# Optimization experiments

Hardware: AMD Instinct MI355X
Metric: run time of the kernel (lower is better)

## Reference

```python
import jax, jax.numpy as jnp
import numpy as np
import math

PS = 65          # patch_size
NB_ANG = 8       # num_ang_bins
NB_SP = 4        # num_spatial_bins
CLIP = 0.2
EPS = 1e-10
BIN_KS = 2 * (PS // (NB_SP + 1))   # 26
BIN_STRIDE = PS // NB_SP           # 16
BIN_PAD = BIN_KS // 4              # 6


def _gaussian_kernel2d(ks, sigma):
    x = jnp.arange(ks, dtype=jnp.float32) - ks // 2
    if ks % 2 == 0:
        x = x + 0.5
    g = jnp.exp(-(x * x) / (2.0 * sigma * sigma))
    g = g / g.sum()
    return jnp.outer(g, g)  # [ps, ps]


def _sift_pooling_kernel(ks):
    ks2 = ks / 2.0
    xc2 = ks2 - jnp.abs(jnp.arange(ks, dtype=jnp.float32) + 0.5 - ks2)
    return jnp.outer(xc2, xc2) / (ks2 * ks2)  # [26, 26] triangular bilinear kernel


def _l2n(x):
    # torch F.normalize(p=2, dim=-1, eps=1e-12)
    return x / jnp.maximum(jnp.linalg.norm(x, axis=-1, keepdims=True), 1e-12)


def setup_inputs() -> dict:
    key = jax.random.key(0)
    image_batch = jax.random.uniform(key, (16, 3, 520, 520), dtype=jnp.float32)
    return {"image_batch": image_batch}


def reference(image_batch):
    B, C, H, W = image_batch.shape
    nH, nW = H // PS, W // PS
    # torch unfold(2,ps,ps).unfold(3,ps,ps).reshape(-1, c, ps, ps)
    # (row-major reshape replicated exactly, including its channel/patch mixing)
    p = image_batch.reshape(B, C, nH, PS, nW, PS).transpose(0, 1, 2, 4, 3, 5)
    x = p.reshape(-1, C, PS, PS)  # [N, C, ps, ps]; (N,C) treated as independent patches
    N = x.shape[0]

    # kornia spatial_gradient(mode='diff', normalized=True): replicate pad, central diff / 2
    xp = jnp.pad(x, ((0, 0), (0, 0), (1, 1), (1, 1)), mode='edge')
    gx = (xp[:, :, 1:-1, 2:] - xp[:, :, 1:-1, :-2]) * 0.5
    gy = (xp[:, :, 2:, 1:-1] - xp[:, :, :-2, 1:-1]) * 0.5

    mag = jnp.sqrt(gx * gx + gy * gy + EPS)
    ori = jnp.arctan2(gy, gx + EPS) + 2.0 * jnp.pi
    gk = _gaussian_kernel2d(PS, PS / math.sqrt(2.0))
    mag = mag * gk  # Gaussian spatial weighting

    # soft orientation binning
    o_big = (NB_ANG / (2.0 * jnp.pi)) * ori
    bo0f = jnp.floor(o_big)
    wo1 = o_big - bo0f
    bo0 = (bo0f % NB_ANG).astype(jnp.int32)
    bo1 = (bo0 + 1) % NB_ANG
    # [N, C, ps, ps, 8] soft histogram field
    contrib = (jax.nn.one_hot(bo0, NB_ANG, dtype=x.dtype) * ((1.0 - wo1) * mag)[..., None]
               + jax.nn.one_hot(bo1, NB_ANG, dtype=x.dtype) * (wo1 * mag)[..., None])

    # spatial pooling: conv 26x26, stride 16, zero-pad 6 -> 4x4 per angle bin
    contrib = jnp.moveaxis(contrib, -1, 2).reshape(N * C * NB_ANG, 1, PS, PS)
    pk = _sift_pooling_kernel(BIN_KS)[None, None]  # [1,1,26,26]
    pooled = jax.lax.conv_general_dilated(
        contrib, pk,
        window_strides=(BIN_STRIDE, BIN_STRIDE),
        padding=((BIN_PAD, BIN_PAD), (BIN_PAD, BIN_PAD)),
        dimension_numbers=('NCHW', 'OIHW', 'NCHW'))  # [N*C*8, 1, 4, 4]

    desc = pooled.reshape(N, C, NB_ANG * NB_SP * NB_SP)  # [N, C, 128]
    desc = _l2n(desc)
    desc = jnp.clip(desc, 0.0, CLIP)
    desc = _l2n(desc)
    return desc  # [B*nH*nW, C, 128] (root_sift=False)
```

## Files before the change

### kernel.cpp

```cpp
#include <hip/hip_runtime.h>
#include <math.h>

#define PSTR 33

__device__ __forceinline__ float fast_atan2f(float y, float x) {
    float ax = fabsf(x), ay = fabsf(y);
    float mx = fmaxf(ax, ay);
    float mn = fminf(ax, ay);
    float a = mn * __builtin_amdgcn_rcpf(fmaxf(mx, 1e-30f));
    float s = a * a;
    float r = fmaf(s, fmaf(s, fmaf(s, fmaf(s, fmaf(s, -0.0117212f, 0.05265332f),
                    -0.11643287f), 0.19354346f), -0.33262347f), 0.99997726f) * a;
    r = (ay > ax) ? (1.57079637f - r) : r;
    r = (x < 0.0f) ? (3.14159274f - r) : r;
    return copysignf(r, y);
}

#define WGT(SY, RR) ((13.0f - fabsf((float)(RR) - 16.0f * (SY) - 6.5f)) * (1.0f / 13.0f))

#define FMA8(P, W)                                                        \
    P##0 = fmaf(s0, (W), P##0); P##1 = fmaf(s1, (W), P##1);               \
    P##2 = fmaf(s2, (W), P##2); P##3 = fmaf(s3, (W), P##3);               \
    P##4 = fmaf(s4, (W), P##4); P##5 = fmaf(s5, (W), P##5);               \
    P##6 = fmaf(s6, (W), P##6); P##7 = fmaf(s7, (W), P##7);

#define RDL(RR) __uint_as_float((unsigned)__builtin_amdgcn_readlane((int)__float_as_uint(G), (RR)))

#define PIX(ARR, I, RR, ACCUM)                                            \
    {                                                                     \
        float grow = ((RR) < 64) ? RDL((RR) & 63) : g64;                  \
        float gw = grow * GC;                                             \
        float c64r = c64buf[(RR) + 1];                                    \
        float xc = ARR[I];                                                \
        float xl = __shfl_up(xc, 1, 64);   if (lane == 0)  xl = xc;       \
        float xr = __shfl_down(xc, 1, 64); if (lane == 63) xr = c64r;     \
        float dx = xr - xl;                                               \
        float dy = ARR[(I) + 1] - ARR[(I) - 1];                           \
        float magw = sqrtf(fmaf(dx, dx, fmaf(dy, dy, 4e-10f))) * gw;      \
        float ang = fast_atan2f(dy, dx + 2e-10f);                         \
        float o = fmaf(ang, 1.27323954f, 8.0f);                           \
        int bi = (int)o;                                                  \
        float wo1 = o - (float)bi;                                        \
        int bn0 = bi & 7;                                                 \
        int bn1 = (bi + 1) & 7;                                           \
        float q1 = wo1 * magw;                                            \
        float q0 = magw - q1;                                             \
        float s0 = (bn0 == 0) ? q0 : ((bn1 == 0) ? q1 : 0.0f);            \
        float s1 = (bn0 == 1) ? q0 : ((bn1 == 1) ? q1 : 0.0f);            \
        float s2 = (bn0 == 2) ? q0 : ((bn1 == 2) ? q1 : 0.0f);            \
        float s3 = (bn0 == 3) ? q0 : ((bn1 == 3) ? q1 : 0.0f);            \
        float s4 = (bn0 == 4) ? q0 : ((bn1 == 4) ? q1 : 0.0f);            \
        float s5 = (bn0 == 5) ? q0 : ((bn1 == 5) ? q1 : 0.0f);            \
        float s6 = (bn0 == 6) ? q0 : ((bn1 == 6) ? q1 : 0.0f);            \
        float s7 = (bn0 == 7) ? q0 : ((bn1 == 7) ? q1 : 0.0f);            \
        ACCUM                                                             \
    }

#define LOAD_RA(BASE)                                                     \
    _Pragma("unroll")                                                     \
    for (int i = 0; i < 18; ++i) {                                        \
        int rr = (BASE) + i; rr = (rr < 0) ? 0 : ((rr > 64) ? 64 : rr);   \
        RA[i] = src[rr * 520 + lane];                                     \
    }
#define LOAD_RB(BASE)                                                     \
    _Pragma("unroll")                                                     \
    for (int i = 0; i < 19; ++i) {                                        \
        int rr = (BASE) + i; rr = (rr < 0) ? 0 : ((rr > 64) ? 64 : rr);   \
        RB[i] = src[rr * 520 + lane];                                     \
    }
#define PIN_RA  _Pragma("unroll") for (int i = 0; i < 18; ++i) asm volatile("" : "+v"(RA[i]));
#define PIN_RB  _Pragma("unroll") for (int i = 0; i < 19; ++i) asm volatile("" : "+v"(RB[i]));

__global__ __launch_bounds__(64)
__attribute__((amdgpu_waves_per_eu(2, 3)))
void sift_kernel(const float* __restrict__ in, float* __restrict__ out) {
    __shared__ float part[65 * PSTR];
    __shared__ float c64buf[67];

    const int lane = threadIdx.x;
    const int m  = blockIdx.x;
    const int bc = m >> 6;
    const int ij = m & 63;
    const float* src = in + (size_t)bc * (520 * 520) + (ij >> 3) * (65 * 520) + (ij & 7) * 65;

    {
        int rr = lane - 1; rr = (rr < 0) ? 0 : rr;
        c64buf[lane] = src[rr * 520 + 64];
        if (lane < 3) {
            int r2 = 63 + lane; r2 = (r2 > 64) ? 64 : r2;
            c64buf[64 + lane] = src[r2 * 520 + 64];
        }
        if (lane < 32) part[64 * PSTR + lane] = 0.0f;
    }
    float xl63  = src[lane * 520 + 63];
    float xl63b = src[64 * 520 + 63];

    float RA[18], RB[19];
    LOAD_RA(-1)
    LOAD_RB(15)

    float dd = (float)(lane - 32);
    float E  = __expf(-(dd * dd) * (1.0f / 4225.0f));
    float ssum = E;
    #pragma unroll
    for (int off = 32; off > 0; off >>= 1) ssum += __shfl_xor(ssum, off, 64);
    const float e64 = __expf(-1024.0f / 4225.0f);
    float inv = 1.0f / (ssum + e64);
    float G   = E * inv;
    float g64 = e64 * inv;
    const float GC = 0.5f * G;

    const int cb = lane * PSTR;

    float A0=0,A1=0,A2=0,A3=0,A4=0,A5=0,A6=0,A7=0;
    float B0=0,B1=0,B2=0,B3=0,B4=0,B5=0,B6=0,B7=0;
    float C0=0,C1=0,C2=0,C3=0,C4=0,C5=0,C6=0,C7=0;
    float F0=0,F1=0,F2=0,F3=0,F4=0,F5=0,F6=0,F7=0;

    PIN_RA
    #pragma unroll
    for (int r = 0; r < 10; ++r)   PIX(RA, r + 1, r, FMA8(A, WGT(0, r)))
    #pragma unroll
    for (int r = 10; r < 16; ++r)  PIX(RA, r + 1, r, FMA8(A, WGT(0, r)) FMA8(B, WGT(1, r)))

    LOAD_RA(31)
    PIN_RB
    #pragma unroll
    for (int r = 16; r < 20; ++r)  PIX(RB, r - 15, r, FMA8(A, WGT(0, r)) FMA8(B, WGT(1, r)))
    #pragma unroll
    for (int r = 20; r < 26; ++r)  PIX(RB, r - 15, r, FMA8(B, WGT(1, r)))
    #pragma unroll
    for (int r = 26; r < 32; ++r)  PIX(RB, r - 15, r, FMA8(B, WGT(1, r)) FMA8(C, WGT(2, r)))
    part[cb + 0] = A0; part[cb + 1] = A1; part[cb + 2] = A2; part[cb + 3] = A3;
    part[cb + 4] = A4; part[cb + 5] = A5; part[cb + 6] = A6; part[cb + 7] = A7;

    LOAD_RB(47)
    PIN_RA
    #pragma unroll
    for (int r = 32; r < 36; ++r)  PIX(RA, r - 31, r, FMA8(B, WGT(1, r)) FMA8(C, WGT(2, r)))
    #pragma unroll
    for (int r = 36; r < 42; ++r)  PIX(RA, r - 31, r, FMA8(C, WGT(2, r)))
    #pragma unroll
    for (int r = 42; r < 48; ++r)  PIX(RA, r - 31, r, FMA8(C, WGT(2, r)) FMA8(F, WGT(3, r)))
    part[cb + 8] = B0; part[cb + 9] = B1; part[cb +10] = B2; part[cb +11] = B3;
    part[cb +12] = B4; part[cb +13] = B5; part[cb +14] = B6; part[cb +15] = B7;

    PIN_RB
    #pragma unroll
    for (int r = 48; r < 52; ++r)  PIX(RB, r - 47, r, FMA8(C, WGT(2, r)) FMA8(F, WGT(3, r)))
    #pragma unroll
    for (int r = 52; r < 65; ++r)  PIX(RB, r - 47, r, FMA8(F, WGT(3, r)))
    part[cb +16] = C0; part[cb +17] = C1; part[cb +18] = C2; part[cb +19] = C3;
    part[cb +20] = C4; part[cb +21] = C5; part[cb +22] = C6; part[cb +23] = C7;
    part[cb +24] = F0; part[cb +25] = F1; part[cb +26] = F2; part[cb +27] = F3;
    part[cb +28] = F4; part[cb +29] = F5; part[cb +30] = F6; part[cb +31] = F7;

    {
        int r = lane;
        float xu  = c64buf[r];
        float xcc = c64buf[r + 1];
        float xd  = c64buf[r + 2];
        float dx = xcc - xl63;
        float dy = xd - xu;
        float magw = sqrtf(fmaf(dx, dx, fmaf(dy, dy, 4e-10f))) * (G * (0.5f * g64));
        float ang = fast_atan2f(dy, dx + 2e-10f);
        float o   = fmaf(ang, 1.27323954f, 8.0f);
        int bi = (int)o;
        float wo1 = o - (float)bi;
        int b0 = bi & 7;
        int b1 = (bi + 1) & 7;
        float q1 = wo1 * magw;
        float q0 = magw - q1;
        float* eb = &part[64 * PSTR];
        int syA = (r + 6) >> 4; if (syA > 3) syA = 3;
        float uA = (float)(r - 16 * syA + 6);
        float wA = (13.0f - fabsf(uA - 12.5f)) * (1.0f / 13.0f);
        atomicAdd(eb + syA * 8 + b0, q0 * wA);
        atomicAdd(eb + syA * 8 + b1, q1 * wA);
        int syB = syA - 1;
        if (syB >= 0) {
            float uB = (float)(r - 16 * syB + 6);
            float wB = (13.0f - fabsf(uB - 12.5f)) * (1.0f / 13.0f);
            if (wB > 0.0f) {
                atomicAdd(eb + syB * 8 + b0, q0 * wB);
                atomicAdd(eb + syB * 8 + b1, q1 * wB);
            }
        }
        if (lane == 0) {
            float xu2  = c64buf[64];
            float xc2  = c64buf[65];
            float xd2  = c64buf[66];
            float dx2 = xc2 - xl63b;
            float dy2 = xd2 - xu2;
            float mg = sqrtf(fmaf(dx2, dx2, fmaf(dy2, dy2, 4e-10f))) * (g64 * (0.5f * g64));
            float an = fast_atan2f(dy2, dx2 + 2e-10f);
            float o2 = fmaf(an, 1.27323954f, 8.0f);
            int bi2 = (int)o2;
            float w1 = o2 - (float)bi2;
            int c0 = bi2 & 7;
            int c1 = (bi2 + 1) & 7;
            float p1 = w1 * mg;
            float p0 = mg - p1;
            const float w64 = 3.5f * (1.0f / 13.0f);
            atomicAdd(eb + 3 * 8 + c0, p0 * w64);
            atomicAdd(eb + 3 * 8 + c1, p1 * w64);
        }
    }

    {
        float v0, v1;
        #pragma unroll
        for (int h = 0; h < 2; ++h) {
            int o  = lane + h * 64;
            int a  = o >> 4;
            int sy = (o >> 2) & 3;
            int sx = o & 3;
            float s = 0.0f;
            #pragma unroll 2
            for (int k = 0; k < 26; ++k) {
                int c = sx * 16 - 6 + k;
                if ((unsigned)c <= 64u) {
                    float wc = (13.0f - fabsf((float)k - 12.5f)) * (1.0f / 13.0f);
                    s = fmaf(wc, part[c * PSTR + sy * 8 + a], s);
                }
            }
            if (h == 0) v0 = s; else v1 = s;
        }
        float ss = v0 * v0 + v1 * v1;
        #pragma unroll
        for (int off = 32; off > 0; off >>= 1) ss += __shfl_xor(ss, off, 64);
        float sc = 1.0f / fmaxf(sqrtf(ss), 1e-12f);
        v0 = fminf(fmaxf(v0 * sc, 0.0f), 0.2f);
        v1 = fminf(fmaxf(v1 * sc, 0.0f), 0.2f);
        ss = v0 * v0 + v1 * v1;
        #pragma unroll
        for (int off = 32; off > 0; off >>= 1) ss += __shfl_xor(ss, off, 64);
        sc = 1.0f / fmaxf(sqrtf(ss), 1e-12f);
        out[(size_t)m * 128 + lane]      = v0 * sc;
        out[(size_t)m * 128 + lane + 64] = v1 * sc;
    }
}

extern "C" void kernel_launch(void* const* d_in, const int* in_sizes, int n_in,
                              void* d_out, int out_size, void* d_ws, size_t ws_size,
                              hipStream_t stream) {
    const float* in = (const float*)d_in[0];
    float* out = (float*)d_out;
    sift_kernel<<<3072, 64, 0, stream>>>(in, out);
}
```

Measured before the change: 49.50 us.

## Split patch rows across two wavefronts per block with shared partial histograms

```diff
diff --git a/kernel.cpp b/kernel.cpp
--- a/kernel.cpp
+++ b/kernel.cpp
@@ -1,7 +1,7 @@
 #include <hip/hip_runtime.h>
 #include <math.h>
 
-#define PSTR 33
+#define PSTR 57
 
 __device__ __forceinline__ float fast_atan2f(float y, float x) {
     float ax = fabsf(x), ay = fabsf(y);
@@ -56,48 +56,49 @@
         ACCUM                                                             \
     }
 
-#define LOAD_RA(BASE)                                                     \
-    _Pragma("unroll")                                                     \
-    for (int i = 0; i < 18; ++i) {                                        \
-        int rr = (BASE) + i; rr = (rr < 0) ? 0 : ((rr > 64) ? 64 : rr);   \
-        RA[i] = src[rr * 520 + lane];                                     \
-    }
-#define LOAD_RB(BASE)                                                     \
-    _Pragma("unroll")                                                     \
-    for (int i = 0; i < 19; ++i) {                                        \
-        int rr = (BASE) + i; rr = (rr < 0) ? 0 : ((rr > 64) ? 64 : rr);   \
-        RB[i] = src[rr * 520 + lane];                                     \
-    }
 #define PIN_RA  _Pragma("unroll") for (int i = 0; i < 18; ++i) asm volatile("" : "+v"(RA[i]));
 #define PIN_RB  _Pragma("unroll") for (int i = 0; i < 19; ++i) asm volatile("" : "+v"(RB[i]));
 
-__global__ __launch_bounds__(64)
-__attribute__((amdgpu_waves_per_eu(2, 3)))
+__global__ __launch_bounds__(128)
+__attribute__((amdgpu_waves_per_eu(4)))
 void sift_kernel(const float* __restrict__ in, float* __restrict__ out) {
     __shared__ float part[65 * PSTR];
     __shared__ float c64buf[67];
-
-    const int lane = threadIdx.x;
+    __shared__ float ssbuf[4];
+
+    const int tid  = threadIdx.x;
+    const int lane = tid & 63;
+    const int wid  = tid >> 6;
     const int m  = blockIdx.x;
     const int bc = m >> 6;
     const int ij = m & 63;
     const float* src = in + (size_t)bc * (520 * 520) + (ij >> 3) * (65 * 520) + (ij & 7) * 65;
 
-    {
-        int rr = lane - 1; rr = (rr < 0) ? 0 : rr;
-        c64buf[lane] = src[rr * 520 + 64];
-        if (lane < 3) {
-            int r2 = 63 + lane; r2 = (r2 > 64) ? 64 : r2;
-            c64buf[64 + lane] = src[r2 * 520 + 64];
-        }
-        if (lane < 32) part[64 * PSTR + lane] = 0.0f;
-    }
-    float xl63  = src[lane * 520 + 63];
-    float xl63b = src[64 * 520 + 63];
+    if (tid < 67) {
+        int rr = tid - 1; rr = (rr < 0) ? 0 : ((rr > 64) ? 64 : rr);
+        c64buf[tid] = src[rr * 520 + 64];
+    }
+    for (int k = tid; k < 65 * 8; k += 128) {
+        part[(k >> 3) * PSTR + 48 + (k & 7)] = 0.0f;
+    }
+    if (tid < 48) part[64 * PSTR + tid] = 0.0f;
+
+    int r63 = wid * 32 + lane; r63 = (r63 > 64) ? 64 : r63;
+    float xl63 = src[r63 * 520 + 63];
 
     float RA[18], RB[19];
-    LOAD_RA(-1)
-    LOAD_RB(15)
+    const int rbA = wid * 32 - 1;
+    const int rbB = wid * 32 + 15;
+    #pragma unroll
+    for (int i = 0; i < 18; ++i) {
+        int rr = rbA + i; rr = (rr < 0) ? 0 : ((rr > 64) ? 64 : rr);
+        RA[i] = src[rr * 520 + lane];
+    }
+    #pragma unroll
+    for (int i = 0; i < 19; ++i) {
+        int rr = rbB + i; rr = (rr < 0) ? 0 : ((rr > 64) ? 64 : rr);
+        RB[i] = src[rr * 520 + lane];
+    }
 
     float dd = (float)(lane - 32);
     float E  = __expf(-(dd * dd) * (1.0f / 4225.0f));
@@ -110,135 +111,127 @@
     float g64 = e64 * inv;
     const float GC = 0.5f * G;
 
-    const int cb = lane * PSTR;
+    __syncthreads();
 
     float A0=0,A1=0,A2=0,A3=0,A4=0,A5=0,A6=0,A7=0;
     float B0=0,B1=0,B2=0,B3=0,B4=0,B5=0,B6=0,B7=0;
     float C0=0,C1=0,C2=0,C3=0,C4=0,C5=0,C6=0,C7=0;
-    float F0=0,F1=0,F2=0,F3=0,F4=0,F5=0,F6=0,F7=0;
-
-    PIN_RA
-    #pragma unroll
-    for (int r = 0; r < 10; ++r)   PIX(RA, r + 1, r, FMA8(A, WGT(0, r)))
-    #pragma unroll
-    for (int r = 10; r < 16; ++r)  PIX(RA, r + 1, r, FMA8(A, WGT(0, r)) FMA8(B, WGT(1, r)))
-
-    LOAD_RA(31)
-    PIN_RB
-    #pragma unroll
-    for (int r = 16; r < 20; ++r)  PIX(RB, r - 15, r, FMA8(A, WGT(0, r)) FMA8(B, WGT(1, r)))
-    #pragma unroll
-    for (int r = 20; r < 26; ++r)  PIX(RB, r - 15, r, FMA8(B, WGT(1, r)))
-    #pragma unroll
-    for (int r = 26; r < 32; ++r)  PIX(RB, r - 15, r, FMA8(B, WGT(1, r)) FMA8(C, WGT(2, r)))
-    part[cb + 0] = A0; part[cb + 1] = A1; part[cb + 2] = A2; part[cb + 3] = A3;
-    part[cb + 4] = A4; part[cb + 5] = A5; part[cb + 6] = A6; part[cb + 7] = A7;
-
-    LOAD_RB(47)
-    PIN_RA
-    #pragma unroll
-    for (int r = 32; r < 36; ++r)  PIX(RA, r - 31, r, FMA8(B, WGT(1, r)) FMA8(C, WGT(2, r)))
-    #pragma unroll
-    for (int r = 36; r < 42; ++r)  PIX(RA, r - 31, r, FMA8(C, WGT(2, r)))
-    #pragma unroll
-    for (int r = 42; r < 48; ++r)  PIX(RA, r - 31, r, FMA8(C, WGT(2, r)) FMA8(F, WGT(3, r)))
-    part[cb + 8] = B0; part[cb + 9] = B1; part[cb +10] = B2; part[cb +11] = B3;
-    part[cb +12] = B4; part[cb +13] = B5; part[cb +14] = B6; part[cb +15] = B7;
-
-    PIN_RB
-    #pragma unroll
-    for (int r = 48; r < 52; ++r)  PIX(RB, r - 47, r, FMA8(C, WGT(2, r)) FMA8(F, WGT(3, r)))
-    #pragma unroll
-    for (int r = 52; r < 65; ++r)  PIX(RB, r - 47, r, FMA8(F, WGT(3, r)))
-    part[cb +16] = C0; part[cb +17] = C1; part[cb +18] = C2; part[cb +19] = C3;
-    part[cb +20] = C4; part[cb +21] = C5; part[cb +22] = C6; part[cb +23] = C7;
-    part[cb +24] = F0; part[cb +25] = F1; part[cb +26] = F2; part[cb +27] = F3;
-    part[cb +28] = F4; part[cb +29] = F5; part[cb +30] = F6; part[cb +31] = F7;
+
+    if (wid == 0) {
+        PIN_RA
+        #pragma unroll
+        for (int r = 0; r < 10; ++r)   PIX(RA, r + 1, r, FMA8(A, WGT(0, r)))
+        #pragma unroll
+        for (int r = 10; r < 16; ++r)  PIX(RA, r + 1, r, FMA8(A, WGT(0, r)) FMA8(B, WGT(1, r)))
+        PIN_RB
+        #pragma unroll
+        for (int r = 16; r < 20; ++r)  PIX(RB, r - 15, r, FMA8(A, WGT(0, r)) FMA8(B, WGT(1, r)))
+        #pragma unroll
+        for (int r = 20; r < 26; ++r)  PIX(RB, r - 15, r, FMA8(B, WGT(1, r)))
+        #pragma unroll
+        for (int r = 26; r < 32; ++r)  PIX(RB, r - 15, r, FMA8(B, WGT(1, r)) FMA8(C, WGT(2, r)))
+    } else {
+        PIN_RA
+        #pragma unroll
+        for (int r = 32; r < 36; ++r)  PIX(RA, r - 31, r, FMA8(A, WGT(1, r)) FMA8(B, WGT(2, r)))
+        #pragma unroll
+        for (int r = 36; r < 42; ++r)  PIX(RA, r - 31, r, FMA8(B, WGT(2, r)))
+        #pragma unroll
+        for (int r = 42; r < 48; ++r)  PIX(RA, r - 31, r, FMA8(B, WGT(2, r)) FMA8(C, WGT(3, r)))
+        PIN_RB
+        #pragma unroll
+        for (int r = 48; r < 52; ++r)  PIX(RB, r - 47, r, FMA8(B, WGT(2, r)) FMA8(C, WGT(3, r)))
+        #pragma unroll
+        for (int r = 52; r < 65; ++r)  PIX(RB, r - 47, r, FMA8(C, WGT(3, r)))
+    }
 
     {
-        int r = lane;
-        float xu  = c64buf[r];
-        float xcc = c64buf[r + 1];
-        float xd  = c64buf[r + 2];
-        float dx = xcc - xl63;
-        float dy = xd - xu;
-        float magw = sqrtf(fmaf(dx, dx, fmaf(dy, dy, 4e-10f))) * (G * (0.5f * g64));
-        float ang = fast_atan2f(dy, dx + 2e-10f);
-        float o   = fmaf(ang, 1.27323954f, 8.0f);
-        int bi = (int)o;
-        float wo1 = o - (float)bi;
-        int b0 = bi & 7;
-        int b1 = (bi + 1) & 7;
-        float q1 = wo1 * magw;
-        float q0 = magw - q1;
-        float* eb = &part[64 * PSTR];
-        int syA = (r + 6) >> 4; if (syA > 3) syA = 3;
-        float uA = (float)(r - 16 * syA + 6);
-        float wA = (13.0f - fabsf(uA - 12.5f)) * (1.0f / 13.0f);
-        atomicAdd(eb + syA * 8 + b0, q0 * wA);
-        atomicAdd(eb + syA * 8 + b1, q1 * wA);
-        int syB = syA - 1;
-        if (syB >= 0) {
-            float uB = (float)(r - 16 * syB + 6);
-            float wB = (13.0f - fabsf(uB - 12.5f)) * (1.0f / 13.0f);
-            if (wB > 0.0f) {
-                atomicAdd(eb + syB * 8 + b0, q0 * wB);
-                atomicAdd(eb + syB * 8 + b1, q1 * wB);
+        const int fb = lane * PSTR + wid * 24;
+        part[fb + 0] = A0; part[fb + 1] = A1; part[fb + 2] = A2; part[fb + 3] = A3;
+        part[fb + 4] = A4; part[fb + 5] = A5; part[fb + 6] = A6; part[fb + 7] = A7;
+        part[fb + 8] = B0; part[fb + 9] = B1; part[fb +10] = B2; part[fb +11] = B3;
+        part[fb +12] = B4; part[fb +13] = B5; part[fb +14] = B6; part[fb +15] = B7;
+        part[fb +16] = C0; part[fb +17] = C1; part[fb +18] = C2; part[fb +19] = C3;
+        part[fb +20] = C4; part[fb +21] = C5; part[fb +22] = C6; part[fb +23] = C7;
+    }
+
+    {
+        const int nr = wid ? 33 : 32;
+        if (lane < nr) {
+            int r = wid * 32 + lane;
+            float xu  = c64buf[r];
+            float xcc = c64buf[r + 1];
+            float xd  = c64buf[r + 2];
+            float gr  = (r < 64) ? RDL(r & 63) : g64;
+            float dx = xcc - xl63;
+            float dy = xd - xu;
+            float magw = sqrtf(fmaf(dx, dx, fmaf(dy, dy, 4e-10f))) * (gr * (0.5f * g64));
+            float ang = fast_atan2f(dy, dx + 2e-10f);
+            float o   = fmaf(ang, 1.27323954f, 8.0f);
+            int bi = (int)o;
+            float wo1 = o - (float)bi;
+            int b0 = bi & 7;
+            int b1 = (bi + 1) & 7;
+            float q1 = wo1 * magw;
+            float q0 = magw - q1;
+            float* eb = &part[64 * PSTR];
+            int syA = (r + 6) >> 4; if (syA > 3) syA = 3;
+            float uA = (float)(r - 16 * syA + 6);
+            float wA = (13.0f - fabsf(uA - 12.5f)) * (1.0f / 13.0f);
+            int baseA = (syA + 2 * wid) * 8;
+            atomicAdd(eb + baseA + b0, q0 * wA);
+            atomicAdd(eb + baseA + b1, q1 * wA);
+            int syB = syA - 1;
+            if (syB >= 0) {
+                float uB = (float)(r - 16 * syB + 6);
+                float wB = (13.0f - fabsf(uB - 12.5f)) * (1.0f / 13.0f);
+                if (wB > 0.0f) {
+                    int baseB = (syB + 2 * wid) * 8;
+                    atomicAdd(eb + baseB + b0, q0 * wB);
+                    atomicAdd(eb + baseB + b1, q1 * wB);
+                }
             }
         }
-        if (lane == 0) {
-            float xu2  = c64buf[64];
-            float xc2  = c64buf[65];
-            float xd2  = c64buf[66];
-            float dx2 = xc2 - xl63b;
-            float dy2 = xd2 - xu2;
-            float mg = sqrtf(fmaf(dx2, dx2, fmaf(dy2, dy2, 4e-10f))) * (g64 * (0.5f * g64));
-            float an = fast_atan2f(dy2, dx2 + 2e-10f);
-            float o2 = fmaf(an, 1.27323954f, 8.0f);
-            int bi2 = (int)o2;
-            float w1 = o2 - (float)bi2;
-            int c0 = bi2 & 7;
-            int c1 = (bi2 + 1) & 7;
-            float p1 = w1 * mg;
-            float p0 = mg - p1;
-            const float w64 = 3.5f * (1.0f / 13.0f);
-            atomicAdd(eb + 3 * 8 + c0, p0 * w64);
-            atomicAdd(eb + 3 * 8 + c1, p1 * w64);
+    }
+    __syncthreads();
+
+    float v;
+    {
+        int o  = wid * 64 + lane;
+        int a  = o >> 4;
+        int sy = (o >> 2) & 3;
+        int sx = o & 3;
+        int b1s = (sy == 3) ? 40 : sy * 8;
+        int b2s = (sy == 1) ? 24 : ((sy == 2) ? 32 : 48);
+        float s = 0.0f;
+        #pragma unroll 2
+        for (int k = 0; k < 26; ++k) {
+            int c = sx * 16 - 6 + k;
+            if ((unsigned)c <= 64u) {
+                float wc = (13.0f - fabsf((float)k - 12.5f)) * (1.0f / 13.0f);
+                float pv = part[c * PSTR + b1s + a] + part[c * PSTR + b2s + a];
+                s = fmaf(wc, pv, s);
+            }
         }
-    }
-
-    {
-        float v0, v1;
-        #pragma unroll
-        for (int h = 0; h < 2; ++h) {
-            int o  = lane + h * 64;
-            int a  = o >> 4;
-            int sy = (o >> 2) & 3;
-            int sx = o & 3;
-            float s = 0.0f;
-            #pragma unroll 2
-            for (int k = 0; k < 26; ++k) {
-                int c = sx * 16 - 6 + k;
-                if ((unsigned)c <= 64u) {
-                    float wc = (13.0f - fabsf((float)k - 12.5f)) * (1.0f / 13.0f);
-                    s = fmaf(wc, part[c * PSTR + sy * 8 + a], s);
-                }
-            }
-            if (h == 0) v0 = s; else v1 = s;
-        }
-        float ss = v0 * v0 + v1 * v1;
-        #pragma unroll
-        for (int off = 32; off > 0; off >>= 1) ss += __shfl_xor(ss, off, 64);
-        float sc = 1.0f / fmaxf(sqrtf(ss), 1e-12f);
-        v0 = fminf(fmaxf(v0 * sc, 0.0f), 0.2f);
-        v1 = fminf(fmaxf(v1 * sc, 0.0f), 0.2f);
-        ss = v0 * v0 + v1 * v1;
-        #pragma unroll
-        for (int off = 32; off > 0; off >>= 1) ss += __shfl_xor(ss, off, 64);
-        sc = 1.0f / fmaxf(sqrtf(ss), 1e-12f);
-        out[(size_t)m * 128 + lane]      = v0 * sc;
-        out[(size_t)m * 128 + lane + 64] = v1 * sc;
-    }
+        v = s;
+    }
+
+    float ss = v * v;
+    #pragma unroll
+    for (int off = 32; off > 0; off >>= 1) ss += __shfl_xor(ss, off, 64);
+    if (lane == 0) ssbuf[wid] = ss;
+    __syncthreads();
+    float sst = ssbuf[0] + ssbuf[1];
+    float sc = 1.0f / fmaxf(sqrtf(sst), 1e-12f);
+    v = fminf(fmaxf(v * sc, 0.0f), 0.2f);
+    ss = v * v;
+    #pragma unroll
+    for (int off = 32; off > 0; off >>= 1) ss += __shfl_xor(ss, off, 64);
+    if (lane == 0) ssbuf[2 + wid] = ss;
+    __syncthreads();
+    sst = ssbuf[2] + ssbuf[3];
+    sc = 1.0f / fmaxf(sqrtf(sst), 1e-12f);
+    out[(size_t)m * 128 + wid * 64 + lane] = v * sc;
 }
 
 extern "C" void kernel_launch(void* const* d_in, const int* in_sizes, int n_in,
@@ -246,5 +239,5 @@
                               hipStream_t stream) {
     const float* in = (const float*)d_in[0];
     float* out = (float*)d_out;
-    sift_kernel<<<3072, 64, 0, stream>>>(in, out);
+    sift_kernel<<<3072, 128, 0, stream>>>(in, out);
 }
```

Result: slower. 82.47 us (+66.6%).
